# Kernel optimization log

Hardware: AMD Instinct MI355X
Metric: run time of the kernel (lower is better)

The kernel has to match this reference:

```python
import jax, jax.numpy as jnp
import numpy as np

DIM = 1024
H = 16
DH = DIM // H
SCALE = DH ** -0.5
EPS = 1e-5


def _linear_params(key, fan_in, fan_out):
    k1, k2 = jax.random.split(key)
    bound = 1.0 / np.sqrt(fan_in)
    w = jax.random.uniform(k1, (fan_out, fan_in), jnp.float32, -bound, bound)
    b = jax.random.uniform(k2, (fan_out,), jnp.float32, -bound, bound)
    return w, b


def setup_inputs() -> dict:
    key = jax.random.key(0)
    ks = jax.random.split(key, 16)
    M, K, S_txt, S_img = 32, 128, 1024, 768
    inp = {
        'entity_text': jax.random.normal(ks[0], (M, K, DIM), jnp.float32),
        'entity_image': jax.random.normal(ks[1], (M, K, DIM), jnp.float32),
        'img_feat': jax.random.normal(ks[2], (M, S_img, DIM), jnp.float32),
        'txt_feat': jax.random.normal(ks[3], (M, S_txt, DIM), jnp.float32),
    }
    img_mask = jax.random.randint(ks[4], (M, S_img), 0, 2, jnp.int32)
    txt_mask = jax.random.randint(ks[5], (M, S_txt), 0, 2, jnp.int32)
    # guarantee at least one valid kv token per row (avoids all -inf rows)
    inp['img_mask'] = img_mask.at[:, 0].set(1)
    inp['txt_mask'] = txt_mask.at[:, 0].set(1)
    names = ['wq_t', 'wk_t', 'wv_t', 'wo_t', 'wq_i', 'wk_i', 'wv_i', 'wo_i']
    for i, n in enumerate(names):
        w, b = _linear_params(ks[6 + i], DIM, DIM)
        inp[n] = w
        inp['b' + n[1:]] = b
    inp['g_t'] = jnp.ones((DIM,), jnp.float32)
    inp['beta_t'] = jnp.zeros((DIM,), jnp.float32)
    inp['g_i'] = jnp.ones((DIM,), jnp.float32)
    inp['beta_i'] = jnp.zeros((DIM,), jnp.float32)
    return inp


def _attend(wq, bq, wk, bk, wv, bv, wo, bo, queries, kv, kv_mask):
    M, K, D = queries.shape
    S = kv.shape[1]
    Q = (queries @ wq.T + bq).reshape(M, K, H, DH)
    Kt = (kv @ wk.T + bk).reshape(M, S, H, DH)
    V = (kv @ wv.T + bv).reshape(M, S, H, DH)
    attn = jnp.einsum('mkhd,mshd->mhks', Q, Kt) * SCALE  # [M,H,K,S]
    attn = jnp.where(kv_mask[:, None, None, :] > 0, attn, -jnp.inf)
    attn = jax.nn.softmax(attn, axis=-1)
    attn = jnp.nan_to_num(attn, nan=0.0)  # dropout=eval mode (identity)
    out = jnp.einsum('mhks,mshd->mkhd', attn, V).reshape(M, K, D)
    return out @ wo.T + bo


def _layernorm(x, g, b):
    mu = jnp.mean(x, axis=-1, keepdims=True)
    var = jnp.mean(jnp.square(x - mu), axis=-1, keepdims=True)
    return (x - mu) * jax.lax.rsqrt(var + EPS) * g + b


def reference(entity_text, entity_image, img_feat, txt_feat, img_mask, txt_mask,
              wq_t, bq_t, wk_t, bk_t, wv_t, bv_t, wo_t, bo_t,
              wq_i, bq_i, wk_i, bk_i, wv_i, bv_i, wo_i, bo_i,
              g_t, beta_t, g_i, beta_i):
    out_t = _attend(wq_t, bq_t, wk_t, bk_t, wv_t, bv_t, wo_t, bo_t,
                    entity_text, txt_feat, txt_mask)
    out_i = _attend(wq_i, bq_i, wk_i, bk_i, wv_i, bv_i, wo_i, bo_i,
                    entity_image, img_feat, img_mask)
    et = _layernorm(entity_text + out_t, g_t, beta_t)
    ei = _layernorm(entity_image + out_i, g_i, beta_i)
    return (et, ei)
```

## Files before the change

kernel.cpp:

```cpp
#include <hip/hip_runtime.h>
#include <stdint.h>

typedef unsigned short u16;
typedef __attribute__((ext_vector_type(8))) short short8;
typedef __attribute__((ext_vector_type(4))) float f32x4;

#define SWZ(r) (((r) & 7) << 4)
#define SWZV(dr) ((((dr) & 7) ^ (((dr) >> 3) & 7)) << 4)
#define SCALE 0.125f

__device__ __forceinline__ u16 f2bf(float f) {
  unsigned int x = __float_as_uint(f);
  x += 0x7fffu + ((x >> 16) & 1u);
  return (u16)(x >> 16);
}

__device__ __forceinline__ unsigned int cvtpk_bf16(float lo, float hi) {
  unsigned int r;
  asm("v_cvt_pk_bf16_f32 %0, %1, %2" : "=v"(r) : "v"(lo), "v"(hi));
  return r;
}

__device__ __forceinline__ f32x4 mfma16(short8 a, short8 b, f32x4 c) {
  return __builtin_amdgcn_mfma_f32_16x16x32_bf16(a, b, c, 0, 0, 0);
}

__device__ __forceinline__ void gload_lds16(const u16* g, u16* l) {
  __builtin_amdgcn_global_load_lds(
      (const __attribute__((address_space(1))) unsigned int*)g,
      (__attribute__((address_space(3))) unsigned int*)l, 16, 0, 0);
}

__device__ __forceinline__ int xcd_swz(int bid, int nwg) {
  int cpx = nwg >> 3;
  return (bid & 7) * cpx + (bid >> 3);
}

__device__ __forceinline__ void cvt8(const float* src, u16* dst) {
  f32x4 a = __builtin_nontemporal_load((const f32x4*)src);
  f32x4 b = __builtin_nontemporal_load((const f32x4*)(src + 4));
  uint4 u;
  u.x = cvtpk_bf16(a[0], a[1]);
  u.y = cvtpk_bf16(a[2], a[3]);
  u.z = cvtpk_bf16(b[0], b[1]);
  u.w = cvtpk_bf16(b[2], b[3]);
  *(uint4*)dst = u;
}

__global__ __launch_bounds__(256) void cvt_all_kernel(
    const float* __restrict__ w0, const float* __restrict__ w1,
    const float* __restrict__ w2, const float* __restrict__ w3,
    const float* __restrict__ ent, const float* __restrict__ feat,
    u16* __restrict__ Wbf, u16* __restrict__ entbf, u16* __restrict__ featbf,
    int nE8, int nF8) {
  const int nW8 = 524288;
  int total = nW8 + nE8 + nF8;
  int i = blockIdx.x * 256 + threadIdx.x;
  int stride = gridDim.x * 256;
  for (; i < total; i += stride) {
    if (i < nW8) {
      int mi = i >> 17;
      const float* s = (mi == 0) ? w0 : (mi == 1) ? w1 : (mi == 2) ? w2 : w3;
      size_t off = (size_t)(i & 131071) * 8;
      cvt8(s + off, Wbf + (size_t)mi * 1048576 + off);
    } else if (i < nW8 + nE8) {
      size_t off = (size_t)(i - nW8) * 8;
      cvt8(ent + off, entbf + off);
    } else {
      size_t off = (size_t)(i - nW8 - nE8) * 8;
      cvt8(feat + off, featbf + off);
    }
  }
}

__global__ __launch_bounds__(256) void cvt_a_kernel(
    const float* __restrict__ src, u16* __restrict__ dst, int n8) {
  int i = blockIdx.x * 256 + threadIdx.x;
  int stride = gridDim.x * 256;
  for (; i < n8; i += stride) cvt8(src + (size_t)i * 8, dst + (size_t)i * 8);
}

template <bool OUT_F32>
__device__ __forceinline__ void gemm_core(
    const u16* __restrict__ A, const u16* __restrict__ B,
    const float* __restrict__ bias0, const float* __restrict__ bias1,
    void* __restrict__ Cv, int ldc, int bx, int by, u16* As, u16* Bs) {
  const int tid = threadIdx.x;
  const int lane = tid & 63;
  const int w = tid >> 6;
  const int wr = w >> 1, wc = w & 1;
  const int l15 = lane & 15, lg = lane >> 4;
  const int brow = by * 128;
  const int bcol = bx * 128;

  f32x4 acc[4][4] = {};

  for (int k0 = 0; k0 < 1024; k0 += 64) {
#pragma unroll
    for (int p = 0; p < 4; ++p) {
      int flat = p * 256 + tid;
      int row = flat >> 3;
      int scb = ((flat & 7) * 16) ^ SWZ(row);
      gload_lds16(B + (size_t)(bcol + row) * 1024 + k0 + (scb >> 1),
                  Bs + (size_t)flat * 8);
    }
#pragma unroll
    for (int p = 0; p < 4; ++p) {
      int flat = p * 256 + tid;
      int row = flat >> 3;
      int scb = ((flat & 7) * 16) ^ SWZ(row);
      gload_lds16(A + (size_t)(brow + row) * 1024 + k0 + (scb >> 1),
                  As + (size_t)flat * 8);
    }
    __syncthreads();

    short8 af[4][2], bfr[4][2];
#pragma unroll
    for (int i = 0; i < 4; ++i) {
#pragma unroll
      for (int kk = 0; kk < 2; ++kk) {
        int ar = wr * 64 + i * 16 + l15;
        af[i][kk] = *(const short8*)((const char*)As + ar * 128 +
                                     ((kk * 64 + lg * 16) ^ SWZ(ar)));
        int br = wc * 64 + i * 16 + l15;
        bfr[i][kk] = *(const short8*)((const char*)Bs + br * 128 +
                                      ((kk * 64 + lg * 16) ^ SWZ(br)));
      }
    }
#pragma unroll
    for (int i = 0; i < 4; ++i)
#pragma unroll
      for (int j = 0; j < 4; ++j)
#pragma unroll
        for (int kk = 0; kk < 2; ++kk)
          acc[i][j] = mfma16(af[i][kk], bfr[j][kk], acc[i][j]);
    __syncthreads();
  }

#pragma unroll
  for (int j = 0; j < 4; ++j) {
    int col = bcol + wc * 64 + j * 16 + l15;
    const float* bp = (col < 1024) ? bias0 : bias1;
    float bv = bp[col & 1023];
#pragma unroll
    for (int i = 0; i < 4; ++i) {
      int row0 = brow + wr * 64 + i * 16 + lg * 4;
#pragma unroll
      for (int r = 0; r < 4; ++r) {
        float v = acc[i][j][r] + bv;
        if constexpr (OUT_F32)
          ((float*)Cv)[(size_t)(row0 + r) * ldc + col] = v;
        else
          ((u16*)Cv)[(size_t)(row0 + r) * ldc + col] = f2bf(v);
      }
    }
  }
}

__global__ __launch_bounds__(256, 2) void qkv_gemm_kernel(
    const u16* __restrict__ A0, const u16* __restrict__ B0,
    const float* __restrict__ bq, u16* __restrict__ C0, int gx0, int nwg0,
    const u16* __restrict__ A1, const u16* __restrict__ B1,
    const float* __restrict__ bk, const float* __restrict__ bv,
    u16* __restrict__ C1, int gx1, int nwg1) {
  __shared__ __attribute__((aligned(16))) u16 As[128 * 64];
  __shared__ __attribute__((aligned(16))) u16 Bs[128 * 64];
  int bid = blockIdx.x;
  if (bid < nwg0) {
    int lid = xcd_swz(bid, nwg0);
    gemm_core<false>(A0, B0, bq, bq, C0, 1024, lid % gx0, lid / gx0, As, Bs);
  } else {
    int lid = xcd_swz(bid - nwg0, nwg1);
    gemm_core<false>(A1, B1, bk, bv, C1, 2048, lid % gx1, lid / gx1, As, Bs);
  }
}

__global__ __launch_bounds__(256, 2) void wo2_kernel(
    const u16* __restrict__ A0, const u16* __restrict__ B0,
    const float* __restrict__ b0, float* __restrict__ C0, int n0,
    const u16* __restrict__ A1, const u16* __restrict__ B1,
    const float* __restrict__ b1, float* __restrict__ C1) {
  __shared__ __attribute__((aligned(16))) u16 As[128 * 64];
  __shared__ __attribute__((aligned(16))) u16 Bs[128 * 64];
  int bid = blockIdx.x;
  if (bid < n0) {
    int lid = xcd_swz(bid, n0);
    gemm_core<true>(A0, B0, b0, b0, C0, 1024, lid % 8, lid / 8, As, Bs);
  } else {
    int lid = xcd_swz(bid - n0, gridDim.x - n0);
    gemm_core<true>(A1, B1, b1, b1, C1, 1024, lid % 8, lid / 8, As, Bs);
  }
}

template <bool A_F32, bool OUT_F32>
__global__ __launch_bounds__(256, 2) void gemm_bias_kernel(
    const void* __restrict__ Av, const u16* __restrict__ B,
    const float* __restrict__ bias0, const float* __restrict__ bias1,
    void* __restrict__ Cv, int ldc) {
  __shared__ __attribute__((aligned(16))) u16 As[128 * 64];
  __shared__ __attribute__((aligned(16))) u16 Bs[128 * 64];
  const int tid = threadIdx.x;
  const int nwg = gridDim.x * gridDim.y;
  const int lid = xcd_swz(blockIdx.y * gridDim.x + blockIdx.x, nwg);
  const int bx = lid % gridDim.x;
  const int by = lid / gridDim.x;

  if constexpr (!A_F32) {
    gemm_core<OUT_F32>((const u16*)Av, B, bias0, bias1, Cv, ldc, bx, by, As, Bs);
    return;
  } else {
    const int lane = tid & 63;
    const int w = tid >> 6;
    const int wr = w >> 1, wc = w & 1;
    const int l15 = lane & 15, lg = lane >> 4;
    const int brow = by * 128;
    const int bcol = bx * 128;
    f32x4 acc[4][4] = {};
    for (int k0 = 0; k0 < 1024; k0 += 64) {
#pragma unroll
      for (int p = 0; p < 4; ++p) {
        int flat = p * 256 + tid;
        int row = flat >> 3;
        int scb = ((flat & 7) * 16) ^ SWZ(row);
        gload_lds16(B + (size_t)(bcol + row) * 1024 + k0 + (scb >> 1),
                    Bs + (size_t)flat * 8);
      }
      const float* Af = (const float*)Av;
#pragma unroll
      for (int p = 0; p < 4; ++p) {
        int flat = p * 256 + tid;
        int row = flat >> 3;
        int c8 = flat & 7;
        const float* src = Af + (size_t)(brow + row) * 1024 + k0 + c8 * 8;
        float4 v0 = ((const float4*)src)[0];
        float4 v1 = ((const float4*)src)[1];
        uint4 u;
        u.x = cvtpk_bf16(v0.x, v0.y);
        u.y = cvtpk_bf16(v0.z, v0.w);
        u.z = cvtpk_bf16(v1.x, v1.y);
        u.w = cvtpk_bf16(v1.z, v1.w);
        *(uint4*)((char*)As + row * 128 + ((c8 * 16) ^ SWZ(row))) = u;
      }
      __syncthreads();
      short8 af[4][2], bfr[4][2];
#pragma unroll
      for (int i = 0; i < 4; ++i) {
#pragma unroll
        for (int kk = 0; kk < 2; ++kk) {
          int ar = wr * 64 + i * 16 + l15;
          af[i][kk] = *(const short8*)((const char*)As + ar * 128 +
                                       ((kk * 64 + lg * 16) ^ SWZ(ar)));
          int br = wc * 64 + i * 16 + l15;
          bfr[i][kk] = *(const short8*)((const char*)Bs + br * 128 +
                                        ((kk * 64 + lg * 16) ^ SWZ(br)));
        }
      }
#pragma unroll
      for (int i = 0; i < 4; ++i)
#pragma unroll
        for (int j = 0; j < 4; ++j)
#pragma unroll
          for (int kk = 0; kk < 2; ++kk)
            acc[i][j] = mfma16(af[i][kk], bfr[j][kk], acc[i][j]);
      __syncthreads();
    }
#pragma unroll
    for (int j = 0; j < 4; ++j) {
      int col = bcol + wc * 64 + j * 16 + l15;
      const float* bp = (col < 1024) ? bias0 : bias1;
      float bv = bp[col & 1023];
#pragma unroll
      for (int i = 0; i < 4; ++i) {
        int row0 = brow + wr * 64 + i * 16 + lg * 4;
#pragma unroll
        for (int r = 0; r < 4; ++r) {
          float v = acc[i][j][r] + bv;
          if constexpr (OUT_F32)
            ((float*)Cv)[(size_t)(row0 + r) * ldc + col] = v;
          else
            ((u16*)Cv)[(size_t)(row0 + r) * ldc + col] = f2bf(v);
        }
      }
    }
  }
}

__global__ __launch_bounds__(256, 2) void attn_mfma_kernel(
    const u16* __restrict__ Q, const u16* __restrict__ KV,
    const int* __restrict__ mask, u16* __restrict__ AO, int S, int mbase) {
  __shared__ __attribute__((aligned(16))) u16 Ks[64 * 64];
  __shared__ __attribute__((aligned(16))) u16 Vt[64 * 64];
  __shared__ __attribute__((aligned(16))) u16 Ps[4 * 32 * 64];
  __shared__ float mb[64];

  const int tid = threadIdx.x;
  const int lane = tid & 63;
  const int w = tid >> 6;
  const int lid = xcd_swz(blockIdx.x, gridDim.x);
  const int ml = lid >> 4;
  const int h = lid & 15;
  const int mg = mbase + ml;
  const int l15 = lane & 15, lg = lane >> 4;

  short8 qf[2][2];
#pragma unroll
  for (int qb = 0; qb < 2; ++qb)
#pragma unroll
    for (int kk = 0; kk < 2; ++kk)
      qf[qb][kk] = *(const short8*)(Q + (size_t)(mg * 128 + w * 32 + qb * 16 + l15) * 1024 +
                                    h * 64 + kk * 32 + lg * 8);

  float mrun[2][4], lrun[2][4];
  f32x4 oacc[2][4] = {};
#pragma unroll
  for (int qb = 0; qb < 2; ++qb)
#pragma unroll
    for (int r = 0; r < 4; ++r) {
      mrun[qb][r] = -1e30f;
      lrun[qb][r] = 0.0f;
    }

  const size_t kvbase = (size_t)ml * S * 2048 + h * 64;

  for (int st = 0; st < S; st += 64) {
    if (tid < 64)
      mb[tid] = (mask[(size_t)mg * S + st + tid] > 0) ? 0.0f : -1e30f;
#pragma unroll
    for (int p = 0; p < 2; ++p) {
      int flat = p * 256 + tid;
      int row = flat >> 3;
      int c = flat & 7;
      short8 v = *(const short8*)(KV + kvbase + (size_t)(st + row) * 2048 + c * 8);
      *(short8*)((char*)Ks + row * 128 + ((c * 16) ^ SWZ(row))) = v;
    }
    {
      int sp = (tid >> 3) * 2;
      int c = tid & 7;
      const u16* src = KV + kvbase + 1024 + (size_t)(st + sp) * 2048 + c * 8;
      short8 v0 = *(const short8*)(src);
      short8 v1 = *(const short8*)(src + 2048);
#pragma unroll
      for (int j = 0; j < 8; ++j) {
        int dr = c * 8 + j;
        unsigned int val = (unsigned int)(u16)v0[j] | ((unsigned int)(u16)v1[j] << 16);
        *(unsigned int*)((char*)Vt + dr * 128 + ((sp * 2) ^ SWZV(dr))) = val;
      }
    }
    __syncthreads();

    short8 kf[4][2];
#pragma unroll
    for (int sb = 0; sb < 4; ++sb)
#pragma unroll
      for (int kk = 0; kk < 2; ++kk) {
        int row = sb * 16 + l15;
        kf[sb][kk] = *(const short8*)((const char*)Ks + row * 128 +
                                      ((kk * 64 + lg * 16) ^ SWZ(row)));
      }
    f32x4 sc[2][4] = {};
#pragma unroll
    for (int qb = 0; qb < 2; ++qb)
#pragma unroll
      for (int sb = 0; sb < 4; ++sb)
#pragma unroll
        for (int kk = 0; kk < 2; ++kk)
          sc[qb][sb] = mfma16(qf[qb][kk], kf[sb][kk], sc[qb][sb]);

    float mbv[4];
#pragma unroll
    for (int sb = 0; sb < 4; ++sb) mbv[sb] = mb[sb * 16 + l15];

#pragma unroll
    for (int qb = 0; qb < 2; ++qb) {
#pragma unroll
      for (int r = 0; r < 4; ++r) {
        float s0 = sc[qb][0][r] * SCALE + mbv[0];
        float s1 = sc[qb][1][r] * SCALE + mbv[1];
        float s2 = sc[qb][2][r] * SCALE + mbv[2];
        float s3 = sc[qb][3][r] * SCALE + mbv[3];
        float t = fmaxf(fmaxf(s0, s1), fmaxf(s2, s3));
        for (int d = 1; d < 16; d <<= 1) t = fmaxf(t, __shfl_xor(t, d));
        float mnew = fmaxf(mrun[qb][r], t);
        float resc = __expf(mrun[qb][r] - mnew);
        float p0 = __expf(s0 - mnew);
        float p1 = __expf(s1 - mnew);
        float p2 = __expf(s2 - mnew);
        float p3 = __expf(s3 - mnew);
        float rs = p0 + p1 + p2 + p3;
        for (int d = 1; d < 16; d <<= 1) rs += __shfl_xor(rs, d);
        lrun[qb][r] = lrun[qb][r] * resc + rs;
        mrun[qb][r] = mnew;
#pragma unroll
        for (int db = 0; db < 4; ++db) oacc[qb][db][r] *= resc;
        int row = qb * 16 + lg * 4 + r;
        char* pbase = (char*)Ps + (w * 32 + row) * 128;
        int colb = 2 * l15;
        *(u16*)(pbase + ((0 * 32 + colb) ^ SWZ(row))) = f2bf(p0);
        *(u16*)(pbase + ((1 * 32 + colb) ^ SWZ(row))) = f2bf(p1);
        *(u16*)(pbase + ((2 * 32 + colb) ^ SWZ(row))) = f2bf(p2);
        *(u16*)(pbase + ((3 * 32 + colb) ^ SWZ(row))) = f2bf(p3);
      }
    }
    asm volatile("" ::: "memory");

    short8 pf[2][2], vf[4][2];
#pragma unroll
    for (int qb = 0; qb < 2; ++qb)
#pragma unroll
      for (int kk = 0; kk < 2; ++kk) {
        int row = qb * 16 + l15;
        pf[qb][kk] = *(const short8*)((const char*)Ps + (w * 32 + row) * 128 +
                                      ((kk * 64 + lg * 16) ^ SWZ(row)));
      }
#pragma unroll
    for (int db = 0; db < 4; ++db)
#pragma unroll
      for (int kk = 0; kk < 2; ++kk) {
        int row = db * 16 + l15;
        vf[db][kk] = *(const short8*)((const char*)Vt + row * 128 +
                                      ((kk * 64 + lg * 16) ^ SWZV(row)));
      }
#pragma unroll
    for (int qb = 0; qb < 2; ++qb)
#pragma unroll
      for (int db = 0; db < 4; ++db)
#pragma unroll
        for (int kk = 0; kk < 2; ++kk)
          oacc[qb][db] = mfma16(pf[qb][kk], vf[db][kk], oacc[qb][db]);
    __syncthreads();
  }

#pragma unroll
  for (int qb = 0; qb < 2; ++qb)
#pragma unroll
    for (int db = 0; db < 4; ++db)
#pragma unroll
      for (int r = 0; r < 4; ++r) {
        int grow = mg * 128 + w * 32 + qb * 16 + lg * 4 + r;
        int gcol = h * 64 + db * 16 + l15;
        float v = oacc[qb][db][r] / lrun[qb][r];
        AO[(size_t)grow * 1024 + gcol] = f2bf(v);
      }
}

__device__ __forceinline__ void ln_core(
    const float* __restrict__ X, const float* __restrict__ O,
    const float* __restrict__ g, const float* __restrict__ b,
    float* __restrict__ out, int row) {
  int tid = threadIdx.x;
  const float* xr = X + (size_t)row * 1024;
  const float* orr = O + (size_t)row * 1024;
  float4 xv = *(const float4*)(xr + tid * 4);
  float4 ov = *(const float4*)(orr + tid * 4);
  float v0 = xv.x + ov.x, v1 = xv.y + ov.y, v2 = xv.z + ov.z, v3 = xv.w + ov.w;
  float s = v0 + v1 + v2 + v3;
  float s2 = v0 * v0 + v1 * v1 + v2 * v2 + v3 * v3;
  for (int d = 1; d < 64; d <<= 1) {
    s += __shfl_xor(s, d);
    s2 += __shfl_xor(s2, d);
  }
  __shared__ float ps[4], ps2[4];
  int w = tid >> 6;
  if ((tid & 63) == 0) {
    ps[w] = s;
    ps2[w] = s2;
  }
  __syncthreads();
  s = ps[0] + ps[1] + ps[2] + ps[3];
  s2 = ps2[0] + ps2[1] + ps2[2] + ps2[3];
  float mu = s * (1.0f / 1024.0f);
  float var = s2 * (1.0f / 1024.0f) - mu * mu;
  float rstd = rsqrtf(var + 1e-5f);
  float4 gv = *(const float4*)(g + tid * 4);
  float4 bv = *(const float4*)(b + tid * 4);
  float4 ou;
  ou.x = (v0 - mu) * rstd * gv.x + bv.x;
  ou.y = (v1 - mu) * rstd * gv.y + bv.y;
  ou.z = (v2 - mu) * rstd * gv.z + bv.z;
  ou.w = (v3 - mu) * rstd * gv.w + bv.w;
  *(float4*)(out + (size_t)row * 1024 + tid * 4) = ou;
}

__global__ __launch_bounds__(256) void ln_kernel(
    const float* __restrict__ X, const float* __restrict__ O,
    const float* __restrict__ g, const float* __restrict__ b,
    float* __restrict__ out) {
  ln_core(X, O, g, b, out, blockIdx.x);
}

__global__ __launch_bounds__(256) void ln2_kernel(
    const float* __restrict__ X0, const float* __restrict__ O0,
    const float* __restrict__ g0, const float* __restrict__ b0,
    const float* __restrict__ X1, const float* __restrict__ O1,
    const float* __restrict__ g1, const float* __restrict__ b1,
    float* __restrict__ out) {
  int row = blockIdx.x;
  if (row < 4096)
    ln_core(X0, O0, g0, b0, out, row);
  else
    ln_core(X1, O1, g1, b1, out + 4194304, row - 4096);
}

extern "C" void kernel_launch(void* const* d_in, const int* in_sizes, int n_in,
                              void* d_out, int out_size, void* d_ws, size_t ws_size,
                              hipStream_t stream) {
  const float* ent_t = (const float*)d_in[0];
  const float* ent_i = (const float*)d_in[1];
  const float* img_feat = (const float*)d_in[2];
  const float* txt_feat = (const float*)d_in[3];
  const int* img_mask = (const int*)d_in[4];
  const int* txt_mask = (const int*)d_in[5];
  const float* W[8];
  const float* Bv[8];
  for (int i = 0; i < 8; ++i) {
    W[i] = (const float*)d_in[6 + 2 * i];
    Bv[i] = (const float*)d_in[7 + 2 * i];
  }
  const float* g_t = (const float*)d_in[22];
  const float* beta_t = (const float*)d_in[23];
  const float* g_i = (const float*)d_in[24];
  const float* beta_i = (const float*)d_in[25];
  float* out = (float*)d_out;
  char* ws = (char*)d_ws;

  if (ws_size >= (240ull << 20)) {
    u16* Wbf = (u16*)ws;
    u16* Qbf = (u16*)(ws + (16ull << 20));
    u16* AObf_t = (u16*)(ws + (24ull << 20));
    u16* AObf_i = (u16*)(ws + (32ull << 20));
    u16* entbf = (u16*)(ws + (40ull << 20));
    u16* KVc = (u16*)(ws + (48ull << 20));
    u16* featbf = (u16*)(ws + (176ull << 20));
    float* Of32_t = (float*)(ws + (48ull << 20));
    float* Of32_i = (float*)(ws + (48ull << 20) + (16ull << 20));

    for (int mod = 0; mod < 2; ++mod) {
      const float* ent = mod ? ent_i : ent_t;
      const float* feat = mod ? img_feat : txt_feat;
      const int* msk = mod ? img_mask : txt_mask;
      u16* AObf = mod ? AObf_i : AObf_t;
      int S = mod ? 768 : 1024;
      int crows = 32 * S;

      const u16* wq = Wbf + (size_t)mod * 4 * 1048576;
      const u16* wkv = Wbf + ((size_t)mod * 4 + 1) * 1048576;

      cvt_all_kernel<<<2048, 256, 0, stream>>>(
          W[mod * 4 + 0], W[mod * 4 + 1], W[mod * 4 + 2], W[mod * 4 + 3],
          ent, feat, Wbf + (size_t)mod * 4 * 1048576, entbf, featbf,
          4096 * 128, crows * 128);

      qkv_gemm_kernel<<<256 + 16 * (crows / 128), 256, 0, stream>>>(
          entbf, wq, Bv[mod * 4 + 0], Qbf, 8, 256,
          featbf, wkv, Bv[mod * 4 + 1], Bv[mod * 4 + 2], KVc, 16,
          16 * (crows / 128));

      attn_mfma_kernel<<<512, 256, 0, stream>>>(Qbf, KVc, msk, AObf, S, 0);
    }

    wo2_kernel<<<512, 256, 0, stream>>>(
        AObf_t, Wbf + 3ull * 1048576, Bv[3], Of32_t, 256,
        AObf_i, Wbf + 7ull * 1048576, Bv[7], Of32_i);

    ln2_kernel<<<8192, 256, 0, stream>>>(
        ent_t, Of32_t, g_t, beta_t,
        ent_i, Of32_i, g_i, beta_i, out);
    return;
  }

  int nc = 0;
  size_t Xt = 0;
  for (int t = 1; t <= 4; t <<= 1) {
    size_t x = 134217728ull / t;
    if ((32ull << 20) + x + x / 2 <= ws_size) { nc = t; Xt = x; break; }
  }

  u16* Wbf = (u16*)ws;
  u16* Qbf = (u16*)(ws + (8ull << 20));
  u16* AObf = (u16*)(ws + (16ull << 20));

  if (nc > 0) {
    u16* entbf = (u16*)(ws + (24ull << 20));
    u16* KVc = (u16*)(ws + (32ull << 20));
    u16* featbf = (u16*)(ws + (32ull << 20) + Xt);
    float* Of32 = (float*)(ws + (32ull << 20));
    const int mpc = 32 / nc;

    for (int mod = 0; mod < 2; ++mod) {
      const float* ent = mod ? ent_i : ent_t;
      const float* feat = mod ? img_feat : txt_feat;
      const int* msk = mod ? img_mask : txt_mask;
      int S = mod ? 768 : 1024;
      int crows = mpc * S;

      const u16* wq = Wbf;
      const u16* wkv = Wbf + 1ull * 1048576;
      const u16* wo = Wbf + 3ull * 1048576;

      cvt_all_kernel<<<2048, 256, 0, stream>>>(
          W[mod * 4 + 0], W[mod * 4 + 1], W[mod * 4 + 2], W[mod * 4 + 3],
          ent, feat, Wbf, entbf, featbf, 4096 * 128, crows * 128);

      for (int c = 0; c < nc; ++c) {
        if (c > 0) {
          const float* featc = feat + (size_t)c * mpc * S * 1024;
          cvt_a_kernel<<<2048, 256, 0, stream>>>(featc, featbf, crows * 128);
        }
        int nwg0 = (c == 0) ? 256 : 0;
        int nwg1 = 16 * (crows / 128);
        qkv_gemm_kernel<<<nwg0 + nwg1, 256, 0, stream>>>(
            entbf, wq, Bv[mod * 4 + 0], Qbf, 8, nwg0,
            featbf, wkv, Bv[mod * 4 + 1], Bv[mod * 4 + 2], KVc, 16, nwg1);
        attn_mfma_kernel<<<mpc * 16, 256, 0, stream>>>(Qbf, KVc, msk, AObf, S, c * mpc);
      }

      gemm_bias_kernel<false, true><<<dim3(8, 32), 256, 0, stream>>>(
          AObf, wo, Bv[mod * 4 + 3], Bv[mod * 4 + 3], Of32, 1024);
      ln_kernel<<<4096, 256, 0, stream>>>(ent, Of32,
                                          mod ? g_i : g_t, mod ? beta_i : beta_t,
                                          out + (size_t)mod * 4194304);
    }
  } else {
    int ncf = 4;
    if (ws_size >= (152ull << 20)) ncf = 1;
    else if (ws_size >= (88ull << 20)) ncf = 2;
    u16* KVc = (u16*)(ws + (24ull << 20));
    float* Of32 = (float*)(ws + (24ull << 20));
    const int mpc = 32 / ncf;

    for (int mod = 0; mod < 2; ++mod) {
      const float* ent = mod ? ent_i : ent_t;
      const float* feat = mod ? img_feat : txt_feat;
      const int* msk = mod ? img_mask : txt_mask;
      int S = mod ? 768 : 1024;

      cvt_all_kernel<<<2048, 256, 0, stream>>>(
          W[mod * 4 + 0], W[mod * 4 + 1], W[mod * 4 + 2], W[mod * 4 + 3],
          ent, ent, Wbf, Qbf, Qbf, 0, 0);

      const u16* wq = Wbf;
      const u16* wkv = Wbf + 1ull * 1048576;
      const u16* wo = Wbf + 3ull * 1048576;

      gemm_bias_kernel<true, false><<<dim3(8, 32), 256, 0, stream>>>(
          ent, wq, Bv[mod * 4 + 0], Bv[mod * 4 + 0], Qbf, 1024);

      int crows = mpc * S;
      for (int c = 0; c < ncf; ++c) {
        const float* featc = feat + (size_t)c * mpc * S * 1024;
        gemm_bias_kernel<true, false><<<dim3(16, crows / 128), 256, 0, stream>>>(
            featc, wkv, Bv[mod * 4 + 1], Bv[mod * 4 + 2], KVc, 2048);
        attn_mfma_kernel<<<mpc * 16, 256, 0, stream>>>(Qbf, KVc, msk, AObf, S, c * mpc);
      }

      gemm_bias_kernel<false, true><<<dim3(8, 32), 256, 0, stream>>>(
          AObf, wo, Bv[mod * 4 + 3], Bv[mod * 4 + 3], Of32, 1024);
      ln_kernel<<<4096, 256, 0, stream>>>(ent, Of32,
                                          mod ? g_i : g_t, mod ? beta_i : beta_t,
                                          out + (size_t)mod * 4194304);
    }
  }
}
```

Baseline: 493.1 us.

## Merge text and image attention into one launch with separate KV buffers

Adds a workspace path with separate Q and KV buffers for each modality, so both projections run first and a single attn2_kernel then processes text and image attention together (1024 blocks). This replaces two attention launches of 512 blocks each, which may leave the GPU partly idle at tail and launch boundaries. It requires a larger workspace (400MB), and the path is skipped if the harness provides less.

Result: no change. 499.1 us (+1.2%).

```diff
diff --git a/kernel.cpp b/kernel.cpp
--- a/kernel.cpp
+++ b/kernel.cpp
@@ -285,9 +285,10 @@
   }
 }
 
-__global__ __launch_bounds__(256, 2) void attn_mfma_kernel(
+__device__ __forceinline__ void attn_core(
     const u16* __restrict__ Q, const u16* __restrict__ KV,
-    const int* __restrict__ mask, u16* __restrict__ AO, int S, int mbase) {
+    const int* __restrict__ mask, u16* __restrict__ AO, int S, int mbase,
+    int lid) {
   __shared__ __attribute__((aligned(16))) u16 Ks[64 * 64];
   __shared__ __attribute__((aligned(16))) u16 Vt[64 * 64];
   __shared__ __attribute__((aligned(16))) u16 Ps[4 * 32 * 64];
@@ -296,7 +297,6 @@
   const int tid = threadIdx.x;
   const int lane = tid & 63;
   const int w = tid >> 6;
-  const int lid = xcd_swz(blockIdx.x, gridDim.x);
   const int ml = lid >> 4;
   const int h = lid & 15;
   const int mg = mbase + ml;
@@ -443,6 +443,26 @@
       }
 }
 
+__global__ __launch_bounds__(256, 2) void attn_mfma_kernel(
+    const u16* __restrict__ Q, const u16* __restrict__ KV,
+    const int* __restrict__ mask, u16* __restrict__ AO, int S, int mbase) {
+  int lid = xcd_swz(blockIdx.x, gridDim.x);
+  attn_core(Q, KV, mask, AO, S, mbase, lid);
+}
+
+__global__ __launch_bounds__(256, 2) void attn2_kernel(
+    const u16* __restrict__ Q0, const u16* __restrict__ KV0,
+    const int* __restrict__ m0, u16* __restrict__ AO0, int S0,
+    const u16* __restrict__ Q1, const u16* __restrict__ KV1,
+    const int* __restrict__ m1, u16* __restrict__ AO1, int S1) {
+  int bid = blockIdx.x;
+  if (bid < 512) {
+    attn_core(Q0, KV0, m0, AO0, S0, 0, xcd_swz(bid, 512));
+  } else {
+    attn_core(Q1, KV1, m1, AO1, S1, 0, xcd_swz(bid - 512, 512));
+  }
+}
+
 __device__ __forceinline__ void ln_core(
     const float* __restrict__ X, const float* __restrict__ O,
     const float* __restrict__ g, const float* __restrict__ b,
@@ -523,6 +543,55 @@
   float* out = (float*)d_out;
   char* ws = (char*)d_ws;
 
+  if (ws_size >= (400ull << 20)) {
+    u16* Wbf = (u16*)ws;
+    u16* Qbf_t = (u16*)(ws + (16ull << 20));
+    u16* Qbf_i = (u16*)(ws + (24ull << 20));
+    u16* AObf_t = (u16*)(ws + (32ull << 20));
+    u16* AObf_i = (u16*)(ws + (40ull << 20));
+    u16* entbf = (u16*)(ws + (48ull << 20));
+    u16* KVt = (u16*)(ws + (56ull << 20));
+    u16* KVi = (u16*)(ws + (184ull << 20));
+    u16* featbf = (u16*)(ws + (280ull << 20));
+    float* Of32_t = (float*)(ws + (56ull << 20));
+    float* Of32_i = (float*)(ws + (72ull << 20));
+
+    for (int mod = 0; mod < 2; ++mod) {
+      const float* ent = mod ? ent_i : ent_t;
+      const float* feat = mod ? img_feat : txt_feat;
+      u16* Qbf = mod ? Qbf_i : Qbf_t;
+      u16* KVc = mod ? KVi : KVt;
+      int S = mod ? 768 : 1024;
+      int crows = 32 * S;
+
+      const u16* wq = Wbf + (size_t)mod * 4 * 1048576;
+      const u16* wkv = Wbf + ((size_t)mod * 4 + 1) * 1048576;
+
+      cvt_all_kernel<<<2048, 256, 0, stream>>>(
+          W[mod * 4 + 0], W[mod * 4 + 1], W[mod * 4 + 2], W[mod * 4 + 3],
+          ent, feat, Wbf + (size_t)mod * 4 * 1048576, entbf, featbf,
+          4096 * 128, crows * 128);
+
+      qkv_gemm_kernel<<<256 + 16 * (crows / 128), 256, 0, stream>>>(
+          entbf, wq, Bv[mod * 4 + 0], Qbf, 8, 256,
+          featbf, wkv, Bv[mod * 4 + 1], Bv[mod * 4 + 2], KVc, 16,
+          16 * (crows / 128));
+    }
+
+    attn2_kernel<<<1024, 256, 0, stream>>>(
+        Qbf_t, KVt, txt_mask, AObf_t, 1024,
+        Qbf_i, KVi, img_mask, AObf_i, 768);
+
+    wo2_kernel<<<512, 256, 0, stream>>>(
+        AObf_t, Wbf + 3ull * 1048576, Bv[3], Of32_t, 256,
+        AObf_i, Wbf + 7ull * 1048576, Bv[7], Of32_i);
+
+    ln2_kernel<<<8192, 256, 0, stream>>>(
+        ent_t, Of32_t, g_t, beta_t,
+        ent_i, Of32_i, g_i, beta_i, out);
+    return;
+  }
+
   if (ws_size >= (240ull << 20)) {
     u16* Wbf = (u16*)ws;
     u16* Qbf = (u16*)(ws + (16ull << 20));
```
